# Performance work log

Measured on AMD Instinct MI355X. Metric: run time of the kernel, lower is better.

## Reference

```python
import jax, jax.numpy as jnp
import numpy as np

T, H, E, K, I = 4096, 1024, 8, 2, 2048
EPS = 1e-5


def setup_inputs() -> dict:
    key = jax.random.key(0)
    ks = jax.random.split(key, 5)
    xavier = jax.nn.initializers.variance_scaling(1.0, 'fan_avg', 'uniform', dtype=jnp.float32)
    return {
        'x': jax.random.normal(ks[0], (T, H), dtype=jnp.float32),
        'scale': jnp.ones((H,), dtype=jnp.float32),
        'gate_kernel': xavier(ks[1], (H, E), jnp.float32),
        'gate_bias': jnp.zeros((E,), dtype=jnp.float32),
        'mlp1_weight': xavier(ks[2], (E, 2 * I, H), jnp.float32),
        'mlp1_bias': jnp.zeros((E, 2 * I), dtype=jnp.float32),
        'mlp2_weight': xavier(ks[3], (E, H, I), jnp.float32),
        'mlp2_bias': jnp.zeros((E, H), dtype=jnp.float32),
    }


def reference(x, scale, gate_kernel, gate_bias, mlp1_weight, mlp1_bias, mlp2_weight, mlp2_bias):
    # RMSNorm in fp32
    t = x.astype(jnp.float32)
    rms = jnp.sqrt(jnp.mean(t * t, axis=-1, keepdims=True) + EPS)
    normed = ((t / rms) * scale).astype(x.dtype)  # [T, H]

    # Gating: top-k experts + softmax over selected logits
    gate_logits = normed @ gate_kernel + gate_bias  # [T, E]
    expert_logits, expert_indices = jax.lax.top_k(gate_logits, K)  # [T, K]
    expert_weights = jax.nn.softmax(expert_logits, axis=-1)  # [T, K]

    # Dense all-expert SwiGLU MLP (faithful to vmap-over-experts original)
    # mlp1_weight: [E, 2I, H] -> mlp1: [E, T, 2I]
    mlp1 = jnp.einsum('td,efd->etf', normed, mlp1_weight) + mlp1_bias[:, None, :]
    gate_part = jnp.minimum(mlp1[..., :I], 7.0)
    linear_part = jnp.clip(mlp1[..., I:], -7.0, 7.0)
    swish_gate = gate_part * jax.nn.sigmoid(1.702 * gate_part)
    activated = swish_gate * (linear_part + 1.0)  # [E, T, I]
    # mlp2_weight: [E, H, I] -> expert_outputs: [T, E, H]
    expert_outputs = (jnp.einsum('eti,ehi->eth', activated, mlp2_weight)
                      + mlp2_bias[:, None, :]).transpose(1, 0, 2)

    # Scatter top-k weights to dense [T, E] and combine
    one_hot = jax.nn.one_hot(expert_indices, E, dtype=expert_outputs.dtype)  # [T, K, E]
    dense_gate_weights = jnp.sum(one_hot * expert_weights[..., None], axis=1)  # [T, E]
    fused = jnp.einsum('teh,te->th', expert_outputs, dense_gate_weights)
    return x + fused
```

## Files before the change

kernel.cpp:

```cpp
#include <hip/hip_runtime.h>
#include <hip/hip_bf16.h>
#include <math.h>

#define T_ 4096
#define H_ 1024
#define E_ 8
#define I_ 2048
#define EPS_ 1e-5f
#define LDST 72

using bf16x8 = __attribute__((ext_vector_type(8))) short;
using f32x4  = __attribute__((ext_vector_type(4))) float;

static __device__ __forceinline__ unsigned short f2bf(float f) {
    union { float f; unsigned int u; } v; v.f = f;
    unsigned int u = v.u;
    u += 0x7fffu + ((u >> 16) & 1u);
    return (unsigned short)(u >> 16);
}

__global__ __launch_bounds__(256) void k_convert(
    const float* __restrict__ src, unsigned short* __restrict__ dst)
{
    size_t i = (size_t)blockIdx.x * 256 + threadIdx.x;
    const float4* s = (const float4*)src + i * 2;
    float4 a = s[0], b = s[1];
    ushort4 lo, hi;
    lo.x = f2bf(a.x); lo.y = f2bf(a.y); lo.z = f2bf(a.z); lo.w = f2bf(a.w);
    hi.x = f2bf(b.x); hi.y = f2bf(b.y); hi.z = f2bf(b.z); hi.w = f2bf(b.w);
    ((ushort4*)dst)[i * 2]     = lo;
    ((ushort4*)dst)[i * 2 + 1] = hi;
}

__global__ __launch_bounds__(256) void k_norm_gate(
    const float* __restrict__ x, const float* __restrict__ scale,
    const float* __restrict__ gk, const float* __restrict__ gb,
    unsigned short* __restrict__ normed_bf,
    int* __restrict__ counts, int* __restrict__ tok_list, float* __restrict__ w_list)
{
    int t = blockIdx.x;
    int tid = threadIdx.x;
    int lane = tid & 63, wave = tid >> 6;

    float4 xv = ((const float4*)(x + (size_t)t * H_))[tid];
    float ss = xv.x*xv.x + xv.y*xv.y + xv.z*xv.z + xv.w*xv.w;
    #pragma unroll
    for (int off = 32; off; off >>= 1) ss += __shfl_down(ss, off);

    __shared__ float red[4];
    __shared__ float s_inv;
    if (lane == 0) red[wave] = ss;
    __syncthreads();
    if (tid == 0) {
        float tot = red[0] + red[1] + red[2] + red[3];
        s_inv = 1.0f / sqrtf(tot / (float)H_ + EPS_);
    }
    __syncthreads();
    float inv = s_inv;

    float4 sv = ((const float4*)scale)[tid];
    float nv[4];
    nv[0] = xv.x*inv*sv.x; nv[1] = xv.y*inv*sv.y;
    nv[2] = xv.z*inv*sv.z; nv[3] = xv.w*inv*sv.w;
    ushort4 nb;
    nb.x = f2bf(nv[0]); nb.y = f2bf(nv[1]); nb.z = f2bf(nv[2]); nb.w = f2bf(nv[3]);
    ((ushort4*)(normed_bf + (size_t)t * H_))[tid] = nb;

    float p[E_];
    #pragma unroll
    for (int e = 0; e < E_; e++) p[e] = 0.f;
    int h0 = tid * 4;
    #pragma unroll
    for (int j = 0; j < 4; j++) {
        const float4* g4 = (const float4*)(gk + (size_t)(h0 + j) * E_);
        float4 a = g4[0], b = g4[1];
        float n = nv[j];
        p[0] += n*a.x; p[1] += n*a.y; p[2] += n*a.z; p[3] += n*a.w;
        p[4] += n*b.x; p[5] += n*b.y; p[6] += n*b.z; p[7] += n*b.w;
    }
    __shared__ float pr[E_][4];
    #pragma unroll
    for (int e = 0; e < E_; e++) {
        float v = p[e];
        #pragma unroll
        for (int off = 32; off; off >>= 1) v += __shfl_down(v, off);
        if (lane == 0) pr[e][wave] = v;
    }
    __syncthreads();
    if (tid == 0) {
        float lg[E_];
        #pragma unroll
        for (int e = 0; e < E_; e++)
            lg[e] = pr[e][0] + pr[e][1] + pr[e][2] + pr[e][3] + gb[e];
        int b0 = -1, b1 = -1; float l0 = -1e30f, l1 = -1e30f;
        #pragma unroll
        for (int e = 0; e < E_; e++) {
            if (lg[e] > l0) { l1 = l0; b1 = b0; l0 = lg[e]; b0 = e; }
            else if (lg[e] > l1) { l1 = lg[e]; b1 = e; }
        }
        float e1 = expf(l1 - l0);
        float w0 = 1.f / (1.f + e1);
        float w1 = e1 / (1.f + e1);
        int p0 = atomicAdd(&counts[b0], 1);
        tok_list[b0 * T_ + p0] = t * 2 + 0; w_list[b0 * T_ + p0] = w0;
        int p1 = atomicAdd(&counts[b1], 1);
        tok_list[b1 * T_ + p1] = t * 2 + 1; w_list[b1 * T_ + p1] = w1;
    }
}

__global__ __launch_bounds__(256) void k_init_out(
    const float* __restrict__ x, float* __restrict__ out)
{
    size_t i = (size_t)blockIdx.x * 256 + threadIdx.x;
    ((float4*)out)[i] = ((const float4*)x)[i];
}

template<bool PRE>
__global__ __launch_bounds__(256) void k_mlp1(
    const float* __restrict__ w1f, const unsigned short* __restrict__ w1b,
    const float* __restrict__ b1,
    const unsigned short* __restrict__ normed_bf,
    const int* __restrict__ counts, const int* __restrict__ tok_list,
    unsigned short* __restrict__ act)
{
    int e = blockIdx.z;
    int Ne = counts[e];
    int mt0 = blockIdx.y * 64;
    if (mt0 >= Ne) return;
    int it0 = blockIdx.x * 64;
    int tid = threadIdx.x;
    int lane = tid & 63, wave = tid >> 6;
    int quad = lane >> 4, m16 = lane & 15;

    __shared__ unsigned short lA[64 * LDST];
    __shared__ unsigned short lBg[64 * LDST];
    __shared__ unsigned short lBl[64 * LDST];
    __shared__ int ls_tk[64];

    if (tid < 64) {
        int slot = mt0 + tid;
        ls_tk[tid] = (slot < Ne) ? tok_list[e * T_ + slot] : -1;
    }
    __syncthreads();

    f32x4 accg[4], accl[4];
    #pragma unroll
    for (int ns = 0; ns < 4; ns++) {
        accg[ns] = (f32x4){0.f, 0.f, 0.f, 0.f};
        accl[ns] = (f32x4){0.f, 0.f, 0.f, 0.f};
    }

    const size_t w1base = (size_t)e * 2 * I_ * H_;
    int rA = tid >> 3, sgA = tid & 7;
    int nB = tid >> 2, sgB = tid & 3;

    for (int kk = 0; kk < H_; kk += 64) {
        #pragma unroll
        for (int rr = 0; rr < 64; rr += 32) {
            int r = rA + rr;
            int tk = ls_tk[r];
            uint4 v = make_uint4(0u, 0u, 0u, 0u);
            if (tk >= 0)
                v = *(const uint4*)(normed_bf + (size_t)(tk >> 1) * H_ + kk + sgA * 8);
            *(uint4*)(&lA[r * LDST + sgA * 8]) = v;
        }
        if (PRE) {
            const unsigned short* srcg = w1b + w1base + (size_t)(it0 + nB) * H_ + kk + sgB * 16;
            const unsigned short* srcl = srcg + (size_t)I_ * H_;
            *(uint4*)(&lBg[nB * LDST + sgB * 16])     = ((const uint4*)srcg)[0];
            *(uint4*)(&lBg[nB * LDST + sgB * 16 + 8]) = ((const uint4*)srcg)[1];
            *(uint4*)(&lBl[nB * LDST + sgB * 16])     = ((const uint4*)srcl)[0];
            *(uint4*)(&lBl[nB * LDST + sgB * 16 + 8]) = ((const uint4*)srcl)[1];
        } else {
            const float* srcg = w1f + w1base + (size_t)(it0 + nB) * H_ + kk + sgB * 16;
            const float* srcl = srcg + (size_t)I_ * H_;
            unsigned short tg[16], tl[16];
            #pragma unroll
            for (int q = 0; q < 4; q++) {
                float4 fg = ((const float4*)srcg)[q];
                float4 fl = ((const float4*)srcl)[q];
                tg[q*4+0] = f2bf(fg.x); tg[q*4+1] = f2bf(fg.y);
                tg[q*4+2] = f2bf(fg.z); tg[q*4+3] = f2bf(fg.w);
                tl[q*4+0] = f2bf(fl.x); tl[q*4+1] = f2bf(fl.y);
                tl[q*4+2] = f2bf(fl.z); tl[q*4+3] = f2bf(fl.w);
            }
            *(uint4*)(&lBg[nB * LDST + sgB * 16])     = *(uint4*)(&tg[0]);
            *(uint4*)(&lBg[nB * LDST + sgB * 16 + 8]) = *(uint4*)(&tg[8]);
            *(uint4*)(&lBl[nB * LDST + sgB * 16])     = *(uint4*)(&tl[0]);
            *(uint4*)(&lBl[nB * LDST + sgB * 16 + 8]) = *(uint4*)(&tl[8]);
        }
        __syncthreads();
        #pragma unroll
        for (int ks = 0; ks < 64; ks += 32) {
            bf16x8 af = *(const bf16x8*)(&lA[(wave * 16 + m16) * LDST + ks + quad * 8]);
            #pragma unroll
            for (int ns = 0; ns < 4; ns++) {
                bf16x8 bg = *(const bf16x8*)(&lBg[(ns * 16 + m16) * LDST + ks + quad * 8]);
                accg[ns] = __builtin_amdgcn_mfma_f32_16x16x32_bf16(af, bg, accg[ns], 0, 0, 0);
                bf16x8 bl = *(const bf16x8*)(&lBl[(ns * 16 + m16) * LDST + ks + quad * 8]);
                accl[ns] = __builtin_amdgcn_mfma_f32_16x16x32_bf16(af, bl, accl[ns], 0, 0, 0);
            }
        }
        __syncthreads();
    }

    #pragma unroll
    for (int reg = 0; reg < 4; reg++) {
        int row = wave * 16 + quad * 4 + reg;
        int tk = ls_tk[row];
        if (tk < 0) continue;
        #pragma unroll
        for (int ns = 0; ns < 4; ns++) {
            int i = it0 + ns * 16 + m16;
            float g = accg[ns][reg] + b1[(size_t)e * 2 * I_ + i];
            float l = accl[ns][reg] + b1[(size_t)e * 2 * I_ + I_ + i];
            g = fminf(g, 7.f);
            l = fminf(fmaxf(l, -7.f), 7.f);
            float sw = g / (1.f + expf(-1.702f * g));
            float a = sw * (l + 1.f);
            act[(size_t)tk * I_ + i] = f2bf(a);
        }
    }
}

template<bool PRE>
__global__ __launch_bounds__(256) void k_mlp2(
    const float* __restrict__ w2f, const unsigned short* __restrict__ w2b,
    const float* __restrict__ b2,
    const unsigned short* __restrict__ act,
    const int* __restrict__ counts, const int* __restrict__ tok_list,
    const float* __restrict__ w_list,
    float* __restrict__ out)
{
    int e = blockIdx.z;
    int Ne = counts[e];
    int mt0 = blockIdx.y * 64;
    if (mt0 >= Ne) return;
    int ht0 = blockIdx.x * 64;
    int tid = threadIdx.x;
    int lane = tid & 63, wave = tid >> 6;
    int quad = lane >> 4, m16 = lane & 15;

    __shared__ unsigned short lA[64 * LDST];
    __shared__ unsigned short lB[64 * LDST];
    __shared__ int ls_tk[64];
    __shared__ float ls_w[64];

    if (tid < 64) {
        int slot = mt0 + tid;
        ls_tk[tid] = (slot < Ne) ? tok_list[e * T_ + slot] : -1;
        ls_w[tid]  = (slot < Ne) ? w_list[e * T_ + slot] : 0.f;
    }
    __syncthreads();

    f32x4 acc[4];
    #pragma unroll
    for (int ns = 0; ns < 4; ns++) acc[ns] = (f32x4){0.f, 0.f, 0.f, 0.f};

    const size_t w2base = (size_t)e * H_ * I_;
    int rA = tid >> 3, sgA = tid & 7;
    int nB = tid >> 2, sgB = tid & 3;

    for (int kk = 0; kk < I_; kk += 64) {
        #pragma unroll
        for (int rr = 0; rr < 64; rr += 32) {
            int r = rA + rr;
            int tk = ls_tk[r];
            uint4 v = make_uint4(0u, 0u, 0u, 0u);
            if (tk >= 0)
                v = *(const uint4*)(act + (size_t)tk * I_ + kk + sgA * 8);
            *(uint4*)(&lA[r * LDST + sgA * 8]) = v;
        }
        if (PRE) {
            const unsigned short* src = w2b + w2base + (size_t)(ht0 + nB) * I_ + kk + sgB * 16;
            *(uint4*)(&lB[nB * LDST + sgB * 16])     = ((const uint4*)src)[0];
            *(uint4*)(&lB[nB * LDST + sgB * 16 + 8]) = ((const uint4*)src)[1];
        } else {
            const float* src = w2f + w2base + (size_t)(ht0 + nB) * I_ + kk + sgB * 16;
            unsigned short tb[16];
            #pragma unroll
            for (int q = 0; q < 4; q++) {
                float4 f4 = ((const float4*)src)[q];
                tb[q*4+0] = f2bf(f4.x); tb[q*4+1] = f2bf(f4.y);
                tb[q*4+2] = f2bf(f4.z); tb[q*4+3] = f2bf(f4.w);
            }
            *(uint4*)(&lB[nB * LDST + sgB * 16])     = *(uint4*)(&tb[0]);
            *(uint4*)(&lB[nB * LDST + sgB * 16 + 8]) = *(uint4*)(&tb[8]);
        }
        __syncthreads();
        #pragma unroll
        for (int ks = 0; ks < 64; ks += 32) {
            bf16x8 af = *(const bf16x8*)(&lA[(wave * 16 + m16) * LDST + ks + quad * 8]);
            #pragma unroll
            for (int ns = 0; ns < 4; ns++) {
                bf16x8 bf = *(const bf16x8*)(&lB[(ns * 16 + m16) * LDST + ks + quad * 8]);
                acc[ns] = __builtin_amdgcn_mfma_f32_16x16x32_bf16(af, bf, acc[ns], 0, 0, 0);
            }
        }
        __syncthreads();
    }

    #pragma unroll
    for (int reg = 0; reg < 4; reg++) {
        int row = wave * 16 + quad * 4 + reg;
        int tk = ls_tk[row];
        if (tk < 0) continue;
        int t = tk >> 1;
        float wgt = ls_w[row];
        #pragma unroll
        for (int ns = 0; ns < 4; ns++) {
            int h = ht0 + ns * 16 + m16;
            float v = acc[ns][reg] + b2[(size_t)e * H_ + h];
            atomicAdd(&out[(size_t)t * H_ + h], wgt * v);
        }
    }
}

extern "C" void kernel_launch(void* const* d_in, const int* in_sizes, int n_in,
                              void* d_out, int out_size, void* d_ws, size_t ws_size,
                              hipStream_t stream) {
    const float* x     = (const float*)d_in[0];
    const float* scale = (const float*)d_in[1];
    const float* gk    = (const float*)d_in[2];
    const float* gb    = (const float*)d_in[3];
    const float* w1    = (const float*)d_in[4];
    const float* b1    = (const float*)d_in[5];
    const float* w2    = (const float*)d_in[6];
    const float* b2    = (const float*)d_in[7];
    float* out = (float*)d_out;

    char* ws = (char*)d_ws;
    const size_t MB = 1024 * 1024;
    bool pre = ws_size >= (size_t)138 * MB;

    unsigned short* normed_bf = (unsigned short*)ws;
    unsigned short* act       = (unsigned short*)(ws + 8 * MB);
    unsigned short* w1b = nullptr;
    unsigned short* w2b = nullptr;
    char* ctl;
    if (pre) {
        w1b = (unsigned short*)(ws + 40 * MB);
        w2b = (unsigned short*)(ws + 104 * MB);
        ctl = ws + 136 * MB;
    } else {
        ctl = ws + 40 * MB;
    }
    int*   counts   = (int*)ctl;
    int*   tok_list = (int*)(ctl + 256);
    float* w_list   = (float*)(ctl + 256 + (size_t)E_ * T_ * 4);

    hipMemsetAsync(counts, 0, E_ * sizeof(int), stream);

    k_norm_gate<<<dim3(T_), dim3(256), 0, stream>>>(x, scale, gk, gb,
                                                    normed_bf, counts, tok_list, w_list);
    if (pre) {
        k_convert<<<dim3((E_ * 2 * I_ * H_) / (256 * 8)), dim3(256), 0, stream>>>(w1, w1b);
        k_convert<<<dim3((E_ * H_ * I_) / (256 * 8)), dim3(256), 0, stream>>>(w2, w2b);
    }
    k_init_out<<<dim3(T_ * H_ / (256 * 4)), dim3(256), 0, stream>>>(x, out);

    if (pre) {
        k_mlp1<true><<<dim3(I_ / 64, T_ / 64, E_), dim3(256), 0, stream>>>(
            nullptr, w1b, b1, normed_bf, counts, tok_list, act);
        k_mlp2<true><<<dim3(H_ / 64, T_ / 64, E_), dim3(256), 0, stream>>>(
            nullptr, w2b, b2, act, counts, tok_list, w_list, out);
    } else {
        k_mlp1<false><<<dim3(I_ / 64, T_ / 64, E_), dim3(256), 0, stream>>>(
            w1, nullptr, b1, normed_bf, counts, tok_list, act);
        k_mlp2<false><<<dim3(H_ / 64, T_ / 64, E_), dim3(256), 0, stream>>>(
            w2, nullptr, b2, act, counts, tok_list, w_list, out);
    }
}
```

Baseline: 611.8 us.

## Use 2x2 wave tiling in MLP1 and widen MLP2 tile to 128 columns

MLP1 now arranges its four waves as a 2x2 grid, each computing a 32x32 subtile, so A and B fragments are reused across more MFMAs and LDS reads per MFMA drop. MLP2 widens the output tile from 64 to 128 hidden columns, with each wave computing 32x64, which halves the grid in x and halves how often the gathered activation rows are reloaded. The cost is more accumulator registers and more LDS per MLP2 block, which may lower occupancy, and fewer MLP2 blocks.

After: 603.9 us. No clear change (-1.3%).

```diff
diff --git a/kernel.cpp b/kernel.cpp
--- a/kernel.cpp
+++ b/kernel.cpp
@@ -129,8 +129,9 @@
     if (mt0 >= Ne) return;
     int it0 = blockIdx.x * 64;
     int tid = threadIdx.x;
-    int lane = tid & 63, wave = tid >> 6;
+    int lane = tid & 63, w = tid >> 6;
     int quad = lane >> 4, m16 = lane & 15;
+    int wr = w >> 1, wc = w & 1;
 
     __shared__ unsigned short lA[64 * LDST];
     __shared__ unsigned short lBg[64 * LDST];
@@ -143,12 +144,14 @@
     }
     __syncthreads();
 
-    f32x4 accg[4], accl[4];
-    #pragma unroll
-    for (int ns = 0; ns < 4; ns++) {
-        accg[ns] = (f32x4){0.f, 0.f, 0.f, 0.f};
-        accl[ns] = (f32x4){0.f, 0.f, 0.f, 0.f};
-    }
+    f32x4 accg[2][2], accl[2][2];
+    #pragma unroll
+    for (int mi = 0; mi < 2; mi++)
+        #pragma unroll
+        for (int ni = 0; ni < 2; ni++) {
+            accg[mi][ni] = (f32x4){0.f, 0.f, 0.f, 0.f};
+            accl[mi][ni] = (f32x4){0.f, 0.f, 0.f, 0.f};
+        }
 
     const size_t w1base = (size_t)e * 2 * I_ * H_;
     int rA = tid >> 3, sgA = tid & 7;
@@ -192,33 +195,47 @@
         __syncthreads();
         #pragma unroll
         for (int ks = 0; ks < 64; ks += 32) {
-            bf16x8 af = *(const bf16x8*)(&lA[(wave * 16 + m16) * LDST + ks + quad * 8]);
-            #pragma unroll
-            for (int ns = 0; ns < 4; ns++) {
-                bf16x8 bg = *(const bf16x8*)(&lBg[(ns * 16 + m16) * LDST + ks + quad * 8]);
-                accg[ns] = __builtin_amdgcn_mfma_f32_16x16x32_bf16(af, bg, accg[ns], 0, 0, 0);
-                bf16x8 bl = *(const bf16x8*)(&lBl[(ns * 16 + m16) * LDST + ks + quad * 8]);
-                accl[ns] = __builtin_amdgcn_mfma_f32_16x16x32_bf16(af, bl, accl[ns], 0, 0, 0);
+            bf16x8 af[2], bg[2], bl[2];
+            #pragma unroll
+            for (int mi = 0; mi < 2; mi++)
+                af[mi] = *(const bf16x8*)(&lA[(wr * 32 + mi * 16 + m16) * LDST + ks + quad * 8]);
+            #pragma unroll
+            for (int ni = 0; ni < 2; ni++) {
+                bg[ni] = *(const bf16x8*)(&lBg[(wc * 32 + ni * 16 + m16) * LDST + ks + quad * 8]);
+                bl[ni] = *(const bf16x8*)(&lBl[(wc * 32 + ni * 16 + m16) * LDST + ks + quad * 8]);
             }
+            #pragma unroll
+            for (int mi = 0; mi < 2; mi++)
+                #pragma unroll
+                for (int ni = 0; ni < 2; ni++) {
+                    accg[mi][ni] = __builtin_amdgcn_mfma_f32_16x16x32_bf16(
+                        af[mi], bg[ni], accg[mi][ni], 0, 0, 0);
+                    accl[mi][ni] = __builtin_amdgcn_mfma_f32_16x16x32_bf16(
+                        af[mi], bl[ni], accl[mi][ni], 0, 0, 0);
+                }
         }
         __syncthreads();
     }
 
-    #pragma unroll
-    for (int reg = 0; reg < 4; reg++) {
-        int row = wave * 16 + quad * 4 + reg;
-        int tk = ls_tk[row];
-        if (tk < 0) continue;
-        #pragma unroll
-        for (int ns = 0; ns < 4; ns++) {
-            int i = it0 + ns * 16 + m16;
-            float g = accg[ns][reg] + b1[(size_t)e * 2 * I_ + i];
-            float l = accl[ns][reg] + b1[(size_t)e * 2 * I_ + I_ + i];
-            g = fminf(g, 7.f);
-            l = fminf(fmaxf(l, -7.f), 7.f);
-            float sw = g / (1.f + expf(-1.702f * g));
-            float a = sw * (l + 1.f);
-            act[(size_t)tk * I_ + i] = f2bf(a);
+    const float* b1g = b1 + (size_t)e * 2 * I_;
+    const float* b1l = b1g + I_;
+    #pragma unroll
+    for (int mi = 0; mi < 2; mi++) {
+        #pragma unroll
+        for (int reg = 0; reg < 4; reg++) {
+            int row = wr * 32 + mi * 16 + quad * 4 + reg;
+            int tk = ls_tk[row];
+            if (tk < 0) continue;
+            #pragma unroll
+            for (int ni = 0; ni < 2; ni++) {
+                int i = it0 + wc * 32 + ni * 16 + m16;
+                float g = accg[mi][ni][reg] + b1g[i];
+                float l = accl[mi][ni][reg] + b1l[i];
+                g = fminf(g, 7.f);
+                l = fminf(fmaxf(l, -7.f), 7.f);
+                float sw = g / (1.f + expf(-1.702f * g));
+                act[(size_t)tk * I_ + i] = f2bf(sw * (l + 1.f));
+            }
         }
     }
 }
@@ -236,13 +253,14 @@
     int Ne = counts[e];
     int mt0 = blockIdx.y * 64;
     if (mt0 >= Ne) return;
-    int ht0 = blockIdx.x * 64;
+    int ht0 = blockIdx.x * 128;
     int tid = threadIdx.x;
-    int lane = tid & 63, wave = tid >> 6;
+    int lane = tid & 63, w = tid >> 6;
     int quad = lane >> 4, m16 = lane & 15;
+    int wr = w >> 1, wc = w & 1;
 
     __shared__ unsigned short lA[64 * LDST];
-    __shared__ unsigned short lB[64 * LDST];
+    __shared__ unsigned short lB[128 * LDST];
     __shared__ int ls_tk[64];
     __shared__ float ls_w[64];
 
@@ -253,9 +271,12 @@
     }
     __syncthreads();
 
-    f32x4 acc[4];
-    #pragma unroll
-    for (int ns = 0; ns < 4; ns++) acc[ns] = (f32x4){0.f, 0.f, 0.f, 0.f};
+    f32x4 acc[2][4];
+    #pragma unroll
+    for (int mi = 0; mi < 2; mi++)
+        #pragma unroll
+        for (int ni = 0; ni < 4; ni++)
+            acc[mi][ni] = (f32x4){0.f, 0.f, 0.f, 0.f};
 
     const size_t w2base = (size_t)e * H_ * I_;
     int rA = tid >> 3, sgA = tid & 7;
@@ -271,47 +292,62 @@
                 v = *(const uint4*)(act + (size_t)tk * I_ + kk + sgA * 8);
             *(uint4*)(&lA[r * LDST + sgA * 8]) = v;
         }
-        if (PRE) {
-            const unsigned short* src = w2b + w2base + (size_t)(ht0 + nB) * I_ + kk + sgB * 16;
-            *(uint4*)(&lB[nB * LDST + sgB * 16])     = ((const uint4*)src)[0];
-            *(uint4*)(&lB[nB * LDST + sgB * 16 + 8]) = ((const uint4*)src)[1];
-        } else {
-            const float* src = w2f + w2base + (size_t)(ht0 + nB) * I_ + kk + sgB * 16;
-            unsigned short tb[16];
-            #pragma unroll
-            for (int q = 0; q < 4; q++) {
-                float4 f4 = ((const float4*)src)[q];
-                tb[q*4+0] = f2bf(f4.x); tb[q*4+1] = f2bf(f4.y);
-                tb[q*4+2] = f2bf(f4.z); tb[q*4+3] = f2bf(f4.w);
+        #pragma unroll
+        for (int rr = 0; rr < 128; rr += 64) {
+            int r = nB + rr;
+            if (PRE) {
+                const unsigned short* src = w2b + w2base + (size_t)(ht0 + r) * I_ + kk + sgB * 16;
+                *(uint4*)(&lB[r * LDST + sgB * 16])     = ((const uint4*)src)[0];
+                *(uint4*)(&lB[r * LDST + sgB * 16 + 8]) = ((const uint4*)src)[1];
+            } else {
+                const float* src = w2f + w2base + (size_t)(ht0 + r) * I_ + kk + sgB * 16;
+                unsigned short tb[16];
+                #pragma unroll
+                for (int q = 0; q < 4; q++) {
+                    float4 f4 = ((const float4*)src)[q];
+                    tb[q*4+0] = f2bf(f4.x); tb[q*4+1] = f2bf(f4.y);
+                    tb[q*4+2] = f2bf(f4.z); tb[q*4+3] = f2bf(f4.w);
+                }
+                *(uint4*)(&lB[r * LDST + sgB * 16])     = *(uint4*)(&tb[0]);
+                *(uint4*)(&lB[r * LDST + sgB * 16 + 8]) = *(uint4*)(&tb[8]);
             }
-            *(uint4*)(&lB[nB * LDST + sgB * 16])     = *(uint4*)(&tb[0]);
-            *(uint4*)(&lB[nB * LDST + sgB * 16 + 8]) = *(uint4*)(&tb[8]);
         }
         __syncthreads();
         #pragma unroll
         for (int ks = 0; ks < 64; ks += 32) {
-            bf16x8 af = *(const bf16x8*)(&lA[(wave * 16 + m16) * LDST + ks + quad * 8]);
-            #pragma unroll
-            for (int ns = 0; ns < 4; ns++) {
-                bf16x8 bf = *(const bf16x8*)(&lB[(ns * 16 + m16) * LDST + ks + quad * 8]);
-                acc[ns] = __builtin_amdgcn_mfma_f32_16x16x32_bf16(af, bf, acc[ns], 0, 0, 0);
+            bf16x8 af[2], bf[4];
+            #pragma unroll
+            for (int mi = 0; mi < 2; mi++)
+                af[mi] = *(const bf16x8*)(&lA[(wr * 32 + mi * 16 + m16) * LDST + ks + quad * 8]);
+            #pragma unroll
+            for (int ni = 0; ni < 4; ni++)
+                bf[ni] = *(const bf16x8*)(&lB[(wc * 64 + ni * 16 + m16) * LDST + ks + quad * 8]);
+            #pragma unroll
+            for (int mi = 0; mi < 2; mi++)
+                #pragma unroll
+                for (int ni = 0; ni < 4; ni++)
+                    acc[mi][ni] = __builtin_amdgcn_mfma_f32_16x16x32_bf16(
+                        af[mi], bf[ni], acc[mi][ni], 0, 0, 0);
+        }
+        __syncthreads();
+    }
+
+    const float* b2e = b2 + (size_t)e * H_;
+    #pragma unroll
+    for (int mi = 0; mi < 2; mi++) {
+        #pragma unroll
+        for (int reg = 0; reg < 4; reg++) {
+            int row = wr * 32 + mi * 16 + quad * 4 + reg;
+            int tk = ls_tk[row];
+            if (tk < 0) continue;
+            int t = tk >> 1;
+            float wgt = ls_w[row];
+            #pragma unroll
+            for (int ni = 0; ni < 4; ni++) {
+                int h = ht0 + wc * 64 + ni * 16 + m16;
+                float v = acc[mi][ni][reg] + b2e[h];
+                atomicAdd(&out[(size_t)t * H_ + h], wgt * v);
             }
-        }
-        __syncthreads();
-    }
-
-    #pragma unroll
-    for (int reg = 0; reg < 4; reg++) {
-        int row = wave * 16 + quad * 4 + reg;
-        int tk = ls_tk[row];
-        if (tk < 0) continue;
-        int t = tk >> 1;
-        float wgt = ls_w[row];
-        #pragma unroll
-        for (int ns = 0; ns < 4; ns++) {
-            int h = ht0 + ns * 16 + m16;
-            float v = acc[ns][reg] + b2[(size_t)e * H_ + h];
-            atomicAdd(&out[(size_t)t * H_ + h], wgt * v);
         }
     }
 }
@@ -362,12 +398,12 @@
     if (pre) {
         k_mlp1<true><<<dim3(I_ / 64, T_ / 64, E_), dim3(256), 0, stream>>>(
             nullptr, w1b, b1, normed_bf, counts, tok_list, act);
-        k_mlp2<true><<<dim3(H_ / 64, T_ / 64, E_), dim3(256), 0, stream>>>(
+        k_mlp2<true><<<dim3(H_ / 128, T_ / 64, E_), dim3(256), 0, stream>>>(
             nullptr, w2b, b2, act, counts, tok_list, w_list, out);
     } else {
         k_mlp1<false><<<dim3(I_ / 64, T_ / 64, E_), dim3(256), 0, stream>>>(
             w1, nullptr, b1, normed_bf, counts, tok_list, act);
-        k_mlp2<false><<<dim3(H_ / 64, T_ / 64, E_), dim3(256), 0, stream>>>(
+        k_mlp2<false><<<dim3(H_ / 128, T_ / 64, E_), dim3(256), 0, stream>>>(
             w2, nullptr, b2, act, counts, tok_list, w_list, out);
     }
 }
```
